# Performance work log

Measured on AMD Instinct MI355X. Metric: run time of the kernel, lower is better.

## Reference

```python
import jax, jax.numpy as jnp
import numpy as np

N_SRC = 100000   # source nodes (columns of adj)
N_DST = 50000    # target nodes (rows of adj)
N_EDGES = 3200000
N_IN = 256
N_OUT = 128


def setup_inputs() -> dict:
    key = jax.random.key(0)
    k = jax.random.split(key, 7)
    stdv = 1.0 / np.sqrt(N_IN)
    x = jax.random.normal(k[0], (N_SRC, N_IN), dtype=jnp.float32)
    W = jax.random.uniform(k[1], (N_OUT, N_IN), minval=-stdv, maxval=stdv, dtype=jnp.float32)
    b = jax.random.uniform(k[2], (N_OUT,), minval=-stdv, maxval=stdv, dtype=jnp.float32)
    adj_rows = jax.random.randint(k[3], (N_EDGES,), 0, N_DST)
    adj_cols = jax.random.randint(k[4], (N_EDGES,), 0, N_SRC)
    # mean-aggregation-style normalized weights (generic positive values)
    adj_vals = jax.random.uniform(k[5], (N_EDGES,), dtype=jnp.float32)
    previous_index = jax.random.randint(k[6], (N_DST,), 0, N_SRC)
    return {"x": x, "W": W, "b": b, "adj_vals": adj_vals,
            "adj_rows": adj_rows, "adj_cols": adj_cols,
            "previous_index": previous_index}


def reference(x, W, b, adj_vals, adj_rows, adj_cols, previous_index):
    # linear projection: h = x @ W.T + b            -> [N_SRC, n_out]
    h = jnp.einsum('ni,oi->no', x, W) + b
    # spmm(adj, h) via COO gather + segment-sum      -> [N_DST, n_out]
    msgs = adj_vals[:, None] * h[adj_cols]          # [E, n_out]
    support = jax.ops.segment_sum(msgs, adj_rows, num_segments=previous_index.shape[0])
    # gather self features and concat                -> [N_DST, 2*n_out]
    return jnp.concatenate([h[previous_index], support], axis=1)
```

## Files before the change

### kernel.cpp

```cpp
#include <hip/hip_runtime.h>
#include <hip/hip_bf16.h>

#define N_IN      256
#define N_OUTC    128
#define RPS       512
#define RPS_SHIFT 9
#define TILE      4096
#define EPT       16
#define SPILL_CAP 8192

typedef __attribute__((ext_vector_type(8))) short bf16x8;
typedef __attribute__((ext_vector_type(4))) float f32x4;
typedef unsigned short ushort_t;
typedef unsigned int uint_t;

__device__ inline unsigned short f2bf(float f) {
    unsigned u = __float_as_uint(f);
    unsigned r = u + 0x7fffu + ((u >> 16) & 1u);
    return (unsigned short)(r >> 16);
}
__device__ inline float bf_lo(uint_t g) { return __uint_as_float(g << 16); }
__device__ inline float bf_hi(uint_t g) { return __uint_as_float(g & 0xFFFF0000u); }

__global__ void cvtW_kernel(const float* __restrict__ W, ushort_t* __restrict__ wb, int n) {
    int i = blockIdx.x * blockDim.x + threadIdx.x;
    if (i < n) wb[i] = f2bf(W[i]);
}

__global__ __launch_bounds__(256) void gemm_h_kernel(const float* __restrict__ x,
                                                     const ushort_t* __restrict__ wb,
                                                     const float* __restrict__ b,
                                                     ushort_t* __restrict__ h16, int M) {
    const int wave = threadIdx.x >> 6;
    const int lane = threadIdx.x & 63;
    const int quad = lane >> 4;
    const int l16  = lane & 15;
    const int m0   = blockIdx.x * 16;
    const int colbase = wave * 32;

    f32x4 acc0 = {0.f, 0.f, 0.f, 0.f};
    f32x4 acc1 = {0.f, 0.f, 0.f, 0.f};

    const float* xrow = x + (size_t)(m0 + l16) * N_IN + quad * 8;
    const ushort_t* w0 = wb + (size_t)(colbase + l16) * N_IN + quad * 8;
    const ushort_t* w1 = w0 + 16 * N_IN;

    #pragma unroll
    for (int kb = 0; kb < N_IN; kb += 32) {
        float4 a0 = *(const float4*)(xrow + kb);
        float4 a1 = *(const float4*)(xrow + kb + 4);
        union { bf16x8 v; __hip_bfloat162 h2[4]; } u;
        u.h2[0] = __float22bfloat162_rn(make_float2(a0.x, a0.y));
        u.h2[1] = __float22bfloat162_rn(make_float2(a0.z, a0.w));
        u.h2[2] = __float22bfloat162_rn(make_float2(a1.x, a1.y));
        u.h2[3] = __float22bfloat162_rn(make_float2(a1.z, a1.w));
        bf16x8 bf0 = *(const bf16x8*)(w0 + kb);
        bf16x8 bf1 = *(const bf16x8*)(w1 + kb);
        acc0 = __builtin_amdgcn_mfma_f32_16x16x32_bf16(u.v, bf0, acc0, 0, 0, 0);
        acc1 = __builtin_amdgcn_mfma_f32_16x16x32_bf16(u.v, bf1, acc1, 0, 0, 0);
    }

    const int c0 = colbase + l16;
    const int c1 = c0 + 16;
    const float bv0 = b[c0];
    const float bv1 = b[c1];
    ushort_t* hp = h16 + (size_t)(m0 + quad * 4) * N_OUTC;
    #pragma unroll
    for (int r = 0; r < 4; r++) {
        hp[(size_t)r * N_OUTC + c0] = f2bf(acc0[r] + bv0);
        hp[(size_t)r * N_OUTC + c1] = f2bf(acc1[r] + bv1);
    }
}

__global__ __launch_bounds__(256) void buildA_kernel(const int* __restrict__ rows,
                                                     const int* __restrict__ cols,
                                                     const float* __restrict__ vals, int E,
                                                     int* __restrict__ sbCount,
                                                     int2* __restrict__ sbList, int sbCap, int nsb,
                                                     int* __restrict__ spillCnt, int4* __restrict__ spill) {
    __shared__ int cur[256];
    __shared__ int gbase[256];
    const int tid = threadIdx.x;
    const int base = blockIdx.x * TILE;

    for (int i = tid; i < nsb; i += 256) cur[i] = 0;
    __syncthreads();

    int ex[EPT]; int evb[EPT]; int esb[EPT]; int erk[EPT];
    #pragma unroll
    for (int k = 0; k < EPT; k++) {
        int e = base + tid + k * 256;
        if (e < E) {
            int r = rows[e], c = cols[e];
            evb[k] = __float_as_int(vals[e]);
            esb[k] = r >> RPS_SHIFT;
            ex[k]  = c | ((r & (RPS - 1)) << 17);
            erk[k] = atomicAdd(&cur[esb[k]], 1);
        } else esb[k] = -1;
    }
    __syncthreads();
    for (int i = tid; i < nsb; i += 256) gbase[i] = atomicAdd(&sbCount[i], cur[i]);
    __syncthreads();

    #pragma unroll
    for (int k = 0; k < EPT; k++) {
        if (esb[k] < 0) continue;
        int pos = gbase[esb[k]] + erk[k];
        if (pos < sbCap) {
            sbList[(size_t)esb[k] * sbCap + pos] = make_int2(ex[k], evb[k]);
        } else {
            int sp = atomicAdd(spillCnt, 1);
            if (sp < SPILL_CAP)
                spill[sp] = make_int4((esb[k] << RPS_SHIFT) + (int)(((uint_t)ex[k]) >> 17),
                                      ex[k] & 0x1FFFF, evb[k], 0);
        }
    }
}

__global__ __launch_bounds__(256) void sbscan_kernel(const int* __restrict__ sbCount, int sbCap,
                                                     int* __restrict__ sbBase, int nsb) {
    __shared__ int a[256], bsh[256];
    int tid = threadIdx.x;
    int v = 0;
    if (tid < nsb) { v = sbCount[tid]; if (v > sbCap) v = sbCap; }
    a[tid] = v; __syncthreads();
    int* src = a; int* dst = bsh;
    for (int off = 1; off < 256; off <<= 1) {
        dst[tid] = src[tid] + ((tid >= off) ? src[tid - off] : 0);
        __syncthreads();
        int* t = src; src = dst; dst = t;
    }
    if (tid < nsb) sbBase[tid] = tid ? src[tid - 1] : 0;
}

__global__ __launch_bounds__(256) void sort_kernel(const int* __restrict__ sbCount,
                                                   const int* __restrict__ sbBase,
                                                   const int2* __restrict__ sbList, int sbCap,
                                                   int2* __restrict__ csr,
                                                   int* __restrict__ rowStart, int* __restrict__ rowCnt,
                                                   int Ndst) {
    __shared__ int hist[RPS];
    __shared__ int scanA[RPS];
    __shared__ int scanB[RPS];
    __shared__ int cur[RPS];
    const int sb  = blockIdx.x;
    const int tid = threadIdx.x;
    int len = sbCount[sb]; if (len > sbCap) len = sbCap;
    const int base = sbBase[sb];
    const int2* lp = sbList + (size_t)sb * sbCap;

    hist[tid] = 0; hist[tid + 256] = 0;
    __syncthreads();
    for (int i = tid; i < len; i += 256) {
        int rl = (int)(((uint_t)lp[i].x) >> 17);
        atomicAdd(&hist[rl], 1);
    }
    __syncthreads();
    scanA[tid] = hist[tid]; scanA[tid + 256] = hist[tid + 256];
    __syncthreads();
    int* src = scanA; int* dst = scanB;
    for (int off = 1; off < RPS; off <<= 1) {
        int i0 = tid, i1 = tid + 256;
        dst[i0] = src[i0] + ((i0 >= off) ? src[i0 - off] : 0);
        dst[i1] = src[i1] + ((i1 >= off) ? src[i1 - off] : 0);
        __syncthreads();
        int* t = src; src = dst; dst = t;
    }
    #pragma unroll
    for (int j = 0; j < 2; j++) {
        int i = tid + j * 256;
        int excl = i ? src[i - 1] : 0;
        cur[i] = excl;
        int r = sb * RPS + i;
        if (r < Ndst) { rowStart[r] = base + excl; rowCnt[r] = hist[i]; }
    }
    __syncthreads();
    for (int i = tid; i < len; i += 256) {
        int2 e = lp[i];
        int rl = (int)(((uint_t)e.x) >> 17);
        int pos = atomicAdd(&cur[rl], 1);
        csr[(size_t)base + pos] = make_int2(e.x & 0x1FFFF, e.y);
    }
}

__global__ __launch_bounds__(256) void spmm_concat_kernel(const ushort_t* __restrict__ h16,
                                                          const int* __restrict__ rowStart,
                                                          const int* __restrict__ rowCnt,
                                                          const int2* __restrict__ csr,
                                                          const int* __restrict__ prev,
                                                          float* __restrict__ out, int Ndst) {
    int r = blockIdx.x * 4 + (threadIdx.x >> 6);
    if (r >= Ndst) return;
    const int lane = threadIdx.x & 63;
    const int cnt = rowCnt[r];
    const int2* bk = csr + rowStart[r];

    float2 acc = {0.f, 0.f};
    int e = 0;
    for (; e + 8 <= cnt; e += 8) {
        int2 c0 = bk[e], c1 = bk[e+1], c2 = bk[e+2], c3 = bk[e+3];
        int2 c4 = bk[e+4], c5 = bk[e+5], c6 = bk[e+6], c7 = bk[e+7];
        uint_t g0 = *(const uint_t*)(h16 + (size_t)c0.x * N_OUTC + 2 * lane);
        uint_t g1 = *(const uint_t*)(h16 + (size_t)c1.x * N_OUTC + 2 * lane);
        uint_t g2 = *(const uint_t*)(h16 + (size_t)c2.x * N_OUTC + 2 * lane);
        uint_t g3 = *(const uint_t*)(h16 + (size_t)c3.x * N_OUTC + 2 * lane);
        uint_t g4 = *(const uint_t*)(h16 + (size_t)c4.x * N_OUTC + 2 * lane);
        uint_t g5 = *(const uint_t*)(h16 + (size_t)c5.x * N_OUTC + 2 * lane);
        uint_t g6 = *(const uint_t*)(h16 + (size_t)c6.x * N_OUTC + 2 * lane);
        uint_t g7 = *(const uint_t*)(h16 + (size_t)c7.x * N_OUTC + 2 * lane);
        float v0 = __int_as_float(c0.y), v1 = __int_as_float(c1.y);
        float v2 = __int_as_float(c2.y), v3 = __int_as_float(c3.y);
        float v4 = __int_as_float(c4.y), v5 = __int_as_float(c5.y);
        float v6 = __int_as_float(c6.y), v7 = __int_as_float(c7.y);
        acc.x += v0 * bf_lo(g0); acc.y += v0 * bf_hi(g0);
        acc.x += v1 * bf_lo(g1); acc.y += v1 * bf_hi(g1);
        acc.x += v2 * bf_lo(g2); acc.y += v2 * bf_hi(g2);
        acc.x += v3 * bf_lo(g3); acc.y += v3 * bf_hi(g3);
        acc.x += v4 * bf_lo(g4); acc.y += v4 * bf_hi(g4);
        acc.x += v5 * bf_lo(g5); acc.y += v5 * bf_hi(g5);
        acc.x += v6 * bf_lo(g6); acc.y += v6 * bf_hi(g6);
        acc.x += v7 * bf_lo(g7); acc.y += v7 * bf_hi(g7);
    }
    for (; e < cnt; e++) {
        int2 cv = bk[e];
        uint_t g = *(const uint_t*)(h16 + (size_t)cv.x * N_OUTC + 2 * lane);
        float v = __int_as_float(cv.y);
        acc.x += v * bf_lo(g); acc.y += v * bf_hi(g);
    }

    int p = prev[r];
    uint_t g = *(const uint_t*)(h16 + (size_t)p * N_OUTC + 2 * lane);
    float2* o = (float2*)(out + (size_t)r * 256);
    o[lane]      = make_float2(bf_lo(g), bf_hi(g));
    o[64 + lane] = make_float2(acc.x, acc.y);
}

__global__ void spill_kernel(const ushort_t* __restrict__ h16, const int4* __restrict__ spill,
                             const int* __restrict__ spillCnt, float* __restrict__ out) {
    int n = *spillCnt; if (n > SPILL_CAP) n = SPILL_CAP;
    int total = n * 64;
    for (int t = blockIdx.x * blockDim.x + threadIdx.x; t < total; t += gridDim.x * blockDim.x) {
        int idx = t >> 6, lane = t & 63;
        int4 s = spill[idx];
        uint_t g = *(const uint_t*)(h16 + (size_t)s.y * N_OUTC + 2 * lane);
        float v = __int_as_float(s.z);
        atomicAdd(&out[(size_t)s.x * 256 + 128 + 2 * lane],     v * bf_lo(g));
        atomicAdd(&out[(size_t)s.x * 256 + 128 + 2 * lane + 1], v * bf_hi(g));
    }
}

__global__ void concat_only_kernel(const ushort_t* __restrict__ h16, const int* __restrict__ prev,
                                   float* __restrict__ out, int Ndst) {
    int t = blockIdx.x * blockDim.x + threadIdx.x;
    int r = t >> 6, lane = t & 63;
    if (r >= Ndst) return;
    uint_t g = *(const uint_t*)(h16 + (size_t)prev[r] * N_OUTC + 2 * lane);
    ((float2*)out)[(size_t)r * 128 + lane] = make_float2(bf_lo(g), bf_hi(g));
}

__global__ void spmm_atomic_kernel(const ushort_t* __restrict__ h16, const int* __restrict__ rows,
                                   const int* __restrict__ cols, const float* __restrict__ vals,
                                   int E, float* __restrict__ out) {
    long long t = (long long)blockIdx.x * blockDim.x + threadIdx.x;
    int e = (int)(t >> 6), lane = (int)(t & 63);
    if (e >= E) return;
    uint_t g = *(const uint_t*)(h16 + (size_t)cols[e] * N_OUTC + 2 * lane);
    float v = vals[e];
    int r = rows[e];
    atomicAdd(&out[(size_t)r * 256 + 128 + 2 * lane],     v * bf_lo(g));
    atomicAdd(&out[(size_t)r * 256 + 128 + 2 * lane + 1], v * bf_hi(g));
}

extern "C" void kernel_launch(void* const* d_in, const int* in_sizes, int n_in,
                              void* d_out, int out_size, void* d_ws, size_t ws_size,
                              hipStream_t stream) {
    const float* x    = (const float*)d_in[0];
    const float* W    = (const float*)d_in[1];
    const float* b    = (const float*)d_in[2];
    const float* vals = (const float*)d_in[3];
    const int*   rows = (const int*)d_in[4];
    const int*   cols = (const int*)d_in[5];
    const int*   prev = (const int*)d_in[6];
    float* out = (float*)d_out;

    const int Nsrc = in_sizes[0] / N_IN;
    const int E    = in_sizes[3];
    const int Ndst = in_sizes[6];
    const int NSB  = (Ndst + RPS - 1) / RPS;
    const int sbCap = E / NSB + 4096;

    char* ws = (char*)d_ws;
    size_t off = 0;
    ushort_t* h16 = (ushort_t*)(ws + off);
    off += (size_t)Nsrc * N_OUTC * sizeof(ushort_t);
    ushort_t* wb = (ushort_t*)(ws + off);
    off += (size_t)N_OUTC * N_IN * sizeof(ushort_t);
    off = (off + 255) & ~(size_t)255;
    int* sbCount  = (int*)(ws + off);
    int* spillCnt = sbCount + NSB;
    size_t memsetBytes = ((size_t)NSB + 1) * sizeof(int);
    off += memsetBytes;
    off = (off + 255) & ~(size_t)255;
    int* sbBase = (int*)(ws + off);
    off += (size_t)NSB * sizeof(int);
    off = (off + 255) & ~(size_t)255;
    int* rowStart = (int*)(ws + off);
    off += (size_t)Ndst * sizeof(int);
    int* rowCnt = (int*)(ws + off);
    off += (size_t)Ndst * sizeof(int);
    off = (off + 255) & ~(size_t)255;
    int4* spill = (int4*)(ws + off);
    off += (size_t)SPILL_CAP * sizeof(int4);
    off = (off + 255) & ~(size_t)255;
    int2* sbList = (int2*)(ws + off);
    off += (size_t)NSB * sbCap * sizeof(int2);
    off = (off + 255) & ~(size_t)255;
    int2* csr = (int2*)(ws + off);
    off += (size_t)E * sizeof(int2);

    cvtW_kernel<<<(N_OUTC * N_IN + 255) / 256, 256, 0, stream>>>(W, wb, N_OUTC * N_IN);
    gemm_h_kernel<<<Nsrc / 16, 256, 0, stream>>>(x, wb, b, h16, Nsrc);

    if (off <= ws_size && NSB <= 256) {
        hipMemsetAsync(sbCount, 0, memsetBytes, stream);
        buildA_kernel<<<(E + TILE - 1) / TILE, 256, 0, stream>>>(rows, cols, vals, E,
                                                                 sbCount, sbList, sbCap, NSB,
                                                                 spillCnt, spill);
        sbscan_kernel<<<1, 256, 0, stream>>>(sbCount, sbCap, sbBase, NSB);
        sort_kernel<<<NSB, 256, 0, stream>>>(sbCount, sbBase, sbList, sbCap,
                                             csr, rowStart, rowCnt, Ndst);
        spmm_concat_kernel<<<(Ndst + 3) / 4, 256, 0, stream>>>(h16, rowStart, rowCnt, csr,
                                                               prev, out, Ndst);
        spill_kernel<<<64, 256, 0, stream>>>(h16, spill, spillCnt, out);
    } else {
        hipMemsetAsync(out, 0, (size_t)out_size * sizeof(float), stream);
        concat_only_kernel<<<((size_t)Ndst * 64 + 255) / 256, 256, 0, stream>>>(h16, prev, out, Ndst);
        spmm_atomic_kernel<<<((size_t)E * 64 + 255) / 256, 256, 0, stream>>>(h16, rows, cols, vals, E, out);
    }
}
```

Measured before the change: 486.8 us.

## Fuse edge bucketing with GEMM launch, shrink row buckets, use shuffle-broadcast CSR loads

Merges the edge-bucketing kernel and the bf16 projection GEMM into one launch, with blocks split by index, so the two independent stages can run side by side. Bucket size drops from 512 to 64 rows, giving 782 buckets, more sort blocks and less per-bucket slack. The sort unrolls its loops four-way. The SpMM loads 64 CSR entries per wave coalesced and broadcasts them with shuffles instead of having every lane reload them. The cost is more global atomics on bucket counters, a larger single-block scan, and more spill risk from the smaller per-bucket capacity margin.

```diff
diff --git a/kernel.cpp b/kernel.cpp
--- a/kernel.cpp
+++ b/kernel.cpp
@@ -3,8 +3,9 @@
 
 #define N_IN      256
 #define N_OUTC    128
-#define RPS       512
-#define RPS_SHIFT 9
+#define RPS       64
+#define RPS_SHIFT 6
+#define NSB_MAX   1024
 #define TILE      4096
 #define EPT       16
 #define SPILL_CAP 8192
@@ -27,15 +28,61 @@
     if (i < n) wb[i] = f2bf(W[i]);
 }
 
-__global__ __launch_bounds__(256) void gemm_h_kernel(const float* __restrict__ x,
-                                                     const ushort_t* __restrict__ wb,
-                                                     const float* __restrict__ b,
-                                                     ushort_t* __restrict__ h16, int M) {
-    const int wave = threadIdx.x >> 6;
-    const int lane = threadIdx.x & 63;
+__global__ __launch_bounds__(256) void fused_build_gemm_kernel(
+        const int* __restrict__ rows, const int* __restrict__ cols,
+        const float* __restrict__ vals, int E,
+        int* __restrict__ sbCount, int2* __restrict__ sbList, int sbCap, int nsb,
+        int* __restrict__ spillCnt, int4* __restrict__ spill, int nbBuild,
+        const float* __restrict__ x, const ushort_t* __restrict__ wb,
+        const float* __restrict__ b, ushort_t* __restrict__ h16) {
+    __shared__ int cur[NSB_MAX];
+    __shared__ int gbase[NSB_MAX];
+    const int tid = threadIdx.x;
+
+    if (blockIdx.x < (uint_t)nbBuild) {
+        const int base = blockIdx.x * TILE;
+        for (int i = tid; i < nsb; i += 256) cur[i] = 0;
+        __syncthreads();
+
+        int ex[EPT], evb[EPT], esb[EPT], erk[EPT];
+        #pragma unroll
+        for (int k = 0; k < EPT; k++) {
+            int e = base + tid + k * 256;
+            if (e < E) {
+                int r = rows[e], c = cols[e];
+                evb[k] = __float_as_int(vals[e]);
+                esb[k] = r >> RPS_SHIFT;
+                ex[k]  = c | ((r & (RPS - 1)) << 17);
+                erk[k] = atomicAdd(&cur[esb[k]], 1);
+            } else esb[k] = -1;
+        }
+        __syncthreads();
+        for (int i = tid; i < nsb; i += 256)
+            gbase[i] = cur[i] ? atomicAdd(&sbCount[i], cur[i]) : 0;
+        __syncthreads();
+
+        #pragma unroll
+        for (int k = 0; k < EPT; k++) {
+            if (esb[k] < 0) continue;
+            int pos = gbase[esb[k]] + erk[k];
+            if (pos < sbCap) {
+                sbList[(size_t)esb[k] * sbCap + pos] = make_int2(ex[k], evb[k]);
+            } else {
+                int sp = atomicAdd(spillCnt, 1);
+                if (sp < SPILL_CAP)
+                    spill[sp] = make_int4((esb[k] << RPS_SHIFT) + (int)(((uint_t)ex[k]) >> 17),
+                                          ex[k] & 0x1FFFF, evb[k], 0);
+            }
+        }
+        return;
+    }
+
+    const int blk  = blockIdx.x - nbBuild;
+    const int wave = tid >> 6;
+    const int lane = tid & 63;
     const int quad = lane >> 4;
     const int l16  = lane & 15;
-    const int m0   = blockIdx.x * 16;
+    const int m0   = blk * 16;
     const int colbase = wave * 32;
 
     f32x4 acc0 = {0.f, 0.f, 0.f, 0.f};
@@ -72,60 +119,15 @@
     }
 }
 
-__global__ __launch_bounds__(256) void buildA_kernel(const int* __restrict__ rows,
-                                                     const int* __restrict__ cols,
-                                                     const float* __restrict__ vals, int E,
-                                                     int* __restrict__ sbCount,
-                                                     int2* __restrict__ sbList, int sbCap, int nsb,
-                                                     int* __restrict__ spillCnt, int4* __restrict__ spill) {
-    __shared__ int cur[256];
-    __shared__ int gbase[256];
-    const int tid = threadIdx.x;
-    const int base = blockIdx.x * TILE;
-
-    for (int i = tid; i < nsb; i += 256) cur[i] = 0;
-    __syncthreads();
-
-    int ex[EPT]; int evb[EPT]; int esb[EPT]; int erk[EPT];
-    #pragma unroll
-    for (int k = 0; k < EPT; k++) {
-        int e = base + tid + k * 256;
-        if (e < E) {
-            int r = rows[e], c = cols[e];
-            evb[k] = __float_as_int(vals[e]);
-            esb[k] = r >> RPS_SHIFT;
-            ex[k]  = c | ((r & (RPS - 1)) << 17);
-            erk[k] = atomicAdd(&cur[esb[k]], 1);
-        } else esb[k] = -1;
-    }
-    __syncthreads();
-    for (int i = tid; i < nsb; i += 256) gbase[i] = atomicAdd(&sbCount[i], cur[i]);
-    __syncthreads();
-
-    #pragma unroll
-    for (int k = 0; k < EPT; k++) {
-        if (esb[k] < 0) continue;
-        int pos = gbase[esb[k]] + erk[k];
-        if (pos < sbCap) {
-            sbList[(size_t)esb[k] * sbCap + pos] = make_int2(ex[k], evb[k]);
-        } else {
-            int sp = atomicAdd(spillCnt, 1);
-            if (sp < SPILL_CAP)
-                spill[sp] = make_int4((esb[k] << RPS_SHIFT) + (int)(((uint_t)ex[k]) >> 17),
-                                      ex[k] & 0x1FFFF, evb[k], 0);
-        }
-    }
-}
-
-__global__ __launch_bounds__(256) void sbscan_kernel(const int* __restrict__ sbCount, int sbCap,
-                                                     int* __restrict__ sbBase, int nsb) {
-    __shared__ int a[256], bsh[256];
+__global__ __launch_bounds__(1024) void sbscan_kernel(const int* __restrict__ sbCount, int sbCap,
+                                                      int* __restrict__ sbBase, int nsb) {
+    __shared__ int a[NSB_MAX], bsh[NSB_MAX];
     int tid = threadIdx.x;
     int v = 0;
     if (tid < nsb) { v = sbCount[tid]; if (v > sbCap) v = sbCap; }
     a[tid] = v; __syncthreads();
     int* src = a; int* dst = bsh;
-    for (int off = 1; off < 256; off <<= 1) {
+    for (int off = 1; off < 1024; off <<= 1) {
         dst[tid] = src[tid] + ((tid >= off) ? src[tid - off] : 0);
         __syncthreads();
         int* t = src; src = dst; dst = t;
@@ -141,44 +143,59 @@
                                                    int Ndst) {
     __shared__ int hist[RPS];
     __shared__ int scanA[RPS];
-    __shared__ int scanB[RPS];
-    __shared__ int cur[RPS];
+    __shared__ int curx[RPS];
     const int sb  = blockIdx.x;
     const int tid = threadIdx.x;
     int len = sbCount[sb]; if (len > sbCap) len = sbCap;
     const int base = sbBase[sb];
     const int2* lp = sbList + (size_t)sb * sbCap;
 
-    hist[tid] = 0; hist[tid + 256] = 0;
+    if (tid < RPS) hist[tid] = 0;
     __syncthreads();
-    for (int i = tid; i < len; i += 256) {
-        int rl = (int)(((uint_t)lp[i].x) >> 17);
-        atomicAdd(&hist[rl], 1);
-    }
+
+    int i = tid;
+    for (; i + 768 < len; i += 1024) {
+        int x0 = lp[i].x, x1 = lp[i + 256].x, x2 = lp[i + 512].x, x3 = lp[i + 768].x;
+        atomicAdd(&hist[((uint_t)x0) >> 17], 1);
+        atomicAdd(&hist[((uint_t)x1) >> 17], 1);
+        atomicAdd(&hist[((uint_t)x2) >> 17], 1);
+        atomicAdd(&hist[((uint_t)x3) >> 17], 1);
+    }
+    for (; i < len; i += 256) atomicAdd(&hist[((uint_t)lp[i].x) >> 17], 1);
     __syncthreads();
-    scanA[tid] = hist[tid]; scanA[tid + 256] = hist[tid + 256];
+
+    if (tid < RPS) scanA[tid] = hist[tid];
     __syncthreads();
-    int* src = scanA; int* dst = scanB;
     for (int off = 1; off < RPS; off <<= 1) {
-        int i0 = tid, i1 = tid + 256;
-        dst[i0] = src[i0] + ((i0 >= off) ? src[i0 - off] : 0);
-        dst[i1] = src[i1] + ((i1 >= off) ? src[i1 - off] : 0);
-        __syncthreads();
-        int* t = src; src = dst; dst = t;
-    }
-    #pragma unroll
-    for (int j = 0; j < 2; j++) {
-        int i = tid + j * 256;
-        int excl = i ? src[i - 1] : 0;
-        cur[i] = excl;
-        int r = sb * RPS + i;
-        if (r < Ndst) { rowStart[r] = base + excl; rowCnt[r] = hist[i]; }
+        int t = 0;
+        if (tid < RPS) t = scanA[tid] + ((tid >= off) ? scanA[tid - off] : 0);
+        __syncthreads();
+        if (tid < RPS) scanA[tid] = t;
+        __syncthreads();
+    }
+    if (tid < RPS) {
+        int excl = tid ? scanA[tid - 1] : 0;
+        curx[tid] = excl;
+        int r = sb * RPS + tid;
+        if (r < Ndst) { rowStart[r] = base + excl; rowCnt[r] = hist[tid]; }
     }
     __syncthreads();
-    for (int i = tid; i < len; i += 256) {
+
+    i = tid;
+    for (; i + 768 < len; i += 1024) {
+        int2 e0 = lp[i], e1 = lp[i + 256], e2 = lp[i + 512], e3 = lp[i + 768];
+        int p0 = atomicAdd(&curx[((uint_t)e0.x) >> 17], 1);
+        int p1 = atomicAdd(&curx[((uint_t)e1.x) >> 17], 1);
+        int p2 = atomicAdd(&curx[((uint_t)e2.x) >> 17], 1);
+        int p3 = atomicAdd(&curx[((uint_t)e3.x) >> 17], 1);
+        csr[(size_t)base + p0] = make_int2(e0.x & 0x1FFFF, e0.y);
+        csr[(size_t)base + p1] = make_int2(e1.x & 0x1FFFF, e1.y);
+        csr[(size_t)base + p2] = make_int2(e2.x & 0x1FFFF, e2.y);
+        csr[(size_t)base + p3] = make_int2(e3.x & 0x1FFFF, e3.y);
+    }
+    for (; i < len; i += 256) {
         int2 e = lp[i];
-        int rl = (int)(((uint_t)e.x) >> 17);
-        int pos = atomicAdd(&cur[rl], 1);
+        int pos = atomicAdd(&curx[((uint_t)e.x) >> 17], 1);
         csr[(size_t)base + pos] = make_int2(e.x & 0x1FFFF, e.y);
     }
 }
@@ -196,36 +213,42 @@
     const int2* bk = csr + rowStart[r];
 
     float2 acc = {0.f, 0.f};
-    int e = 0;
-    for (; e + 8 <= cnt; e += 8) {
-        int2 c0 = bk[e], c1 = bk[e+1], c2 = bk[e+2], c3 = bk[e+3];
-        int2 c4 = bk[e+4], c5 = bk[e+5], c6 = bk[e+6], c7 = bk[e+7];
-        uint_t g0 = *(const uint_t*)(h16 + (size_t)c0.x * N_OUTC + 2 * lane);
-        uint_t g1 = *(const uint_t*)(h16 + (size_t)c1.x * N_OUTC + 2 * lane);
-        uint_t g2 = *(const uint_t*)(h16 + (size_t)c2.x * N_OUTC + 2 * lane);
-        uint_t g3 = *(const uint_t*)(h16 + (size_t)c3.x * N_OUTC + 2 * lane);
-        uint_t g4 = *(const uint_t*)(h16 + (size_t)c4.x * N_OUTC + 2 * lane);
-        uint_t g5 = *(const uint_t*)(h16 + (size_t)c5.x * N_OUTC + 2 * lane);
-        uint_t g6 = *(const uint_t*)(h16 + (size_t)c6.x * N_OUTC + 2 * lane);
-        uint_t g7 = *(const uint_t*)(h16 + (size_t)c7.x * N_OUTC + 2 * lane);
-        float v0 = __int_as_float(c0.y), v1 = __int_as_float(c1.y);
-        float v2 = __int_as_float(c2.y), v3 = __int_as_float(c3.y);
-        float v4 = __int_as_float(c4.y), v5 = __int_as_float(c5.y);
-        float v6 = __int_as_float(c6.y), v7 = __int_as_float(c7.y);
-        acc.x += v0 * bf_lo(g0); acc.y += v0 * bf_hi(g0);
-        acc.x += v1 * bf_lo(g1); acc.y += v1 * bf_hi(g1);
-        acc.x += v2 * bf_lo(g2); acc.y += v2 * bf_hi(g2);
-        acc.x += v3 * bf_lo(g3); acc.y += v3 * bf_hi(g3);
-        acc.x += v4 * bf_lo(g4); acc.y += v4 * bf_hi(g4);
-        acc.x += v5 * bf_lo(g5); acc.y += v5 * bf_hi(g5);
-        acc.x += v6 * bf_lo(g6); acc.y += v6 * bf_hi(g6);
-        acc.x += v7 * bf_lo(g7); acc.y += v7 * bf_hi(g7);
-    }
-    for (; e < cnt; e++) {
-        int2 cv = bk[e];
-        uint_t g = *(const uint_t*)(h16 + (size_t)cv.x * N_OUTC + 2 * lane);
-        float v = __int_as_float(cv.y);
-        acc.x += v * bf_lo(g); acc.y += v * bf_hi(g);
+    for (int bse = 0; bse < cnt; bse += 64) {
+        int idx = bse + lane;
+        int2 my = make_int2(0, 0);
+        if (idx < cnt) my = bk[idx];
+        int m = cnt - bse; if (m > 64) m = 64;
+        int mg = (m + 7) & ~7;
+        for (int j = 0; j < mg; j += 8) {
+            int c0 = __shfl(my.x, j + 0), c1 = __shfl(my.x, j + 1);
+            int c2 = __shfl(my.x, j + 2), c3 = __shfl(my.x, j + 3);
+            int c4 = __shfl(my.x, j + 4), c5 = __shfl(my.x, j + 5);
+            int c6 = __shfl(my.x, j + 6), c7 = __shfl(my.x, j + 7);
+            uint_t g0 = *(const uint_t*)(h16 + (size_t)c0 * N_OUTC + 2 * lane);
+            uint_t g1 = *(const uint_t*)(h16 + (size_t)c1 * N_OUTC + 2 * lane);
+            uint_t g2 = *(const uint_t*)(h16 + (size_t)c2 * N_OUTC + 2 * lane);
+            uint_t g3 = *(const uint_t*)(h16 + (size_t)c3 * N_OUTC + 2 * lane);
+            uint_t g4 = *(const uint_t*)(h16 + (size_t)c4 * N_OUTC + 2 * lane);
+            uint_t g5 = *(const uint_t*)(h16 + (size_t)c5 * N_OUTC + 2 * lane);
+            uint_t g6 = *(const uint_t*)(h16 + (size_t)c6 * N_OUTC + 2 * lane);
+            uint_t g7 = *(const uint_t*)(h16 + (size_t)c7 * N_OUTC + 2 * lane);
+            float v0 = __int_as_float(__shfl(my.y, j + 0));
+            float v1 = __int_as_float(__shfl(my.y, j + 1));
+            float v2 = __int_as_float(__shfl(my.y, j + 2));
+            float v3 = __int_as_float(__shfl(my.y, j + 3));
+            float v4 = __int_as_float(__shfl(my.y, j + 4));
+            float v5 = __int_as_float(__shfl(my.y, j + 5));
+            float v6 = __int_as_float(__shfl(my.y, j + 6));
+            float v7 = __int_as_float(__shfl(my.y, j + 7));
+            acc.x += v0 * bf_lo(g0); acc.y += v0 * bf_hi(g0);
+            acc.x += v1 * bf_lo(g1); acc.y += v1 * bf_hi(g1);
+            acc.x += v2 * bf_lo(g2); acc.y += v2 * bf_hi(g2);
+            acc.x += v3 * bf_lo(g3); acc.y += v3 * bf_hi(g3);
+            acc.x += v4 * bf_lo(g4); acc.y += v4 * bf_hi(g4);
+            acc.x += v5 * bf_lo(g5); acc.y += v5 * bf_hi(g5);
+            acc.x += v6 * bf_lo(g6); acc.y += v6 * bf_hi(g6);
+            acc.x += v7 * bf_lo(g7); acc.y += v7 * bf_hi(g7);
+        }
     }
 
     int p = prev[r];
@@ -249,6 +272,48 @@
     }
 }
 
+__global__ __launch_bounds__(256) void gemm_only_kernel(const float* __restrict__ x,
+                                                        const ushort_t* __restrict__ wb,
+                                                        const float* __restrict__ b,
+                                                        ushort_t* __restrict__ h16) {
+    const int tid  = threadIdx.x;
+    const int wave = tid >> 6;
+    const int lane = tid & 63;
+    const int quad = lane >> 4;
+    const int l16  = lane & 15;
+    const int m0   = blockIdx.x * 16;
+    const int colbase = wave * 32;
+    f32x4 acc0 = {0.f, 0.f, 0.f, 0.f};
+    f32x4 acc1 = {0.f, 0.f, 0.f, 0.f};
+    const float* xrow = x + (size_t)(m0 + l16) * N_IN + quad * 8;
+    const ushort_t* w0 = wb + (size_t)(colbase + l16) * N_IN + quad * 8;
+    const ushort_t* w1 = w0 + 16 * N_IN;
+    #pragma unroll
+    for (int kb = 0; kb < N_IN; kb += 32) {
+        float4 a0 = *(const float4*)(xrow + kb);
+        float4 a1 = *(const float4*)(xrow + kb + 4);
+        union { bf16x8 v; __hip_bfloat162 h2[4]; } u;
+        u.h2[0] = __float22bfloat162_rn(make_float2(a0.x, a0.y));
+        u.h2[1] = __float22bfloat162_rn(make_float2(a0.z, a0.w));
+        u.h2[2] = __float22bfloat162_rn(make_float2(a1.x, a1.y));
+        u.h2[3] = __float22bfloat162_rn(make_float2(a1.z, a1.w));
+        bf16x8 bf0 = *(const bf16x8*)(w0 + kb);
+        bf16x8 bf1 = *(const bf16x8*)(w1 + kb);
+        acc0 = __builtin_amdgcn_mfma_f32_16x16x32_bf16(u.v, bf0, acc0, 0, 0, 0);
+        acc1 = __builtin_amdgcn_mfma_f32_16x16x32_bf16(u.v, bf1, acc1, 0, 0, 0);
+    }
+    const int c0 = colbase + l16;
+    const int c1 = c0 + 16;
+    const float bv0 = b[c0];
+    const float bv1 = b[c1];
+    ushort_t* hp = h16 + (size_t)(m0 + quad * 4) * N_OUTC;
+    #pragma unroll
+    for (int r = 0; r < 4; r++) {
+        hp[(size_t)r * N_OUTC + c0] = f2bf(acc0[r] + bv0);
+        hp[(size_t)r * N_OUTC + c1] = f2bf(acc1[r] + bv1);
+    }
+}
+
 __global__ void concat_only_kernel(const ushort_t* __restrict__ h16, const int* __restrict__ prev,
                                    float* __restrict__ out, int Ndst) {
     int t = blockIdx.x * blockDim.x + threadIdx.x;
@@ -287,7 +352,9 @@
     const int E    = in_sizes[3];
     const int Ndst = in_sizes[6];
     const int NSB  = (Ndst + RPS - 1) / RPS;
-    const int sbCap = E / NSB + 4096;
+    const int sbCap = E / NSB + 516;
+    const int nbBuild = (E + TILE - 1) / TILE;
+    const int gemmBlocks = Nsrc / 16;
 
     char* ws = (char*)d_ws;
     size_t off = 0;
@@ -319,20 +386,20 @@
     off += (size_t)E * sizeof(int2);
 
     cvtW_kernel<<<(N_OUTC * N_IN + 255) / 256, 256, 0, stream>>>(W, wb, N_OUTC * N_IN);
-    gemm_h_kernel<<<Nsrc / 16, 256, 0, stream>>>(x, wb, b, h16, Nsrc);
-
-    if (off <= ws_size && NSB <= 256) {
+
+    if (off <= ws_size && NSB <= NSB_MAX) {
         hipMemsetAsync(sbCount, 0, memsetBytes, stream);
-        buildA_kernel<<<(E + TILE - 1) / TILE, 256, 0, stream>>>(rows, cols, vals, E,
-                                                                 sbCount, sbList, sbCap, NSB,
-                                                                 spillCnt, spill);
-        sbscan_kernel<<<1, 256, 0, stream>>>(sbCount, sbCap, sbBase, NSB);
+        fused_build_gemm_kernel<<<nbBuild + gemmBlocks, 256, 0, stream>>>(
+            rows, cols, vals, E, sbCount, sbList, sbCap, NSB, spillCnt, spill, nbBuild,
+            x, wb, b, h16);
+        sbscan_kernel<<<1, 1024, 0, stream>>>(sbCount, sbCap, sbBase, NSB);
         sort_kernel<<<NSB, 256, 0, stream>>>(sbCount, sbBase, sbList, sbCap,
                                              csr, rowStart, rowCnt, Ndst);
         spmm_concat_kernel<<<(Ndst + 3) / 4, 256, 0, stream>>>(h16, rowStart, rowCnt, csr,
                                                                prev, out, Ndst);
         spill_kernel<<<64, 256, 0, stream>>>(h16, spill, spillCnt, out);
     } else {
+        gemm_only_kernel<<<gemmBlocks, 256, 0, stream>>>(x, wb, b, h16);
         hipMemsetAsync(out, 0, (size_t)out_size * sizeof(float), stream);
         concat_only_kernel<<<((size_t)Ndst * 64 + 255) / 256, 256, 0, stream>>>(h16, prev, out, Ndst);
         spmm_atomic_kernel<<<((size_t)E * 64 + 255) / 256, 256, 0, stream>>>(h16, rows, cols, vals, E, out);
```

New measurement: 437.0 us. 10.2% less time.
